# Optimization experiments

Measured on AMD Instinct MI355X. Metric: run time of the kernel, lower is better.

The kernel has to match this reference:

```python
import jax, jax.numpy as jnp
import numpy as np

N_NODES = 50000

def _gcn_conv(x, W, b, src, dst, n):
    # GCNConv: add self-loops, symmetric normalization D^-1/2 (A+I) D^-1/2, then aggregate X@W
    h = x @ W  # [N, out]
    loop = jnp.arange(n, dtype=src.dtype)
    s = jnp.concatenate([src, loop])
    d = jnp.concatenate([dst, loop])
    deg = jax.ops.segment_sum(jnp.ones_like(d, dtype=h.dtype), d, num_segments=n)  # in-degree incl self-loop (>=1)
    dinv = jax.lax.rsqrt(deg)
    norm = dinv[s] * dinv[d]  # [E+N]
    msg = h[s] * norm[:, None]  # gather + scale
    out = jax.ops.segment_sum(msg, d, num_segments=n)  # scatter-add
    return out + b

def setup_inputs() -> dict:
    key = jax.random.key(0)
    k1, k2, k3, k4, k5 = jax.random.split(key, 5)
    F_IN, HID, CLS, E = 256, 128, 32, 800000
    x = jax.random.normal(k1, (N_NODES, F_IN), dtype=jnp.float32)
    edge_index = jax.random.randint(k2, (2, E), 0, N_NODES, dtype=jnp.int64)
    W1 = jax.random.normal(k3, (F_IN, HID), dtype=jnp.float32) / np.sqrt(F_IN)
    b1 = jnp.zeros((HID,), dtype=jnp.float32)
    W2 = jax.random.normal(k4, (HID, CLS), dtype=jnp.float32) / np.sqrt(HID)
    b2 = jnp.zeros((CLS,), dtype=jnp.float32)
    return {"x": x, "edge_index": edge_index, "W1": W1, "b1": b1, "W2": W2, "b2": b2}

def reference(x, edge_index, W1, b1, W2, b2):
    src, dst = edge_index[0], edge_index[1]
    h = _gcn_conv(x, W1, b1, src, dst, N_NODES)
    h = jax.nn.relu(h)
    h = _gcn_conv(h, W2, b2, src, dst, N_NODES)
    return jax.nn.log_softmax(h, axis=1)
```

## Files before the change

kernel.cpp:

```cpp
#include <hip/hip_runtime.h>

#define N_NODES 50000
#define N_PAD   50176
#define F_IN 256
#define HID 128
#define CLS 32
#define N_EDGE 800000

#define NB    196
#define NPART 196
#define CHUNK 4082
#define GBLKS 782

typedef short bf16x8 __attribute__((ext_vector_type(8)));
typedef short s16x4  __attribute__((ext_vector_type(4)));
typedef short s16x8  __attribute__((ext_vector_type(8)));
typedef float f32x2  __attribute__((ext_vector_type(2)));
typedef float f32x4  __attribute__((ext_vector_type(4)));

static __device__ inline short f2bf(float f) {
    union { float f; unsigned u; } v; v.f = f;
    unsigned r = v.u + 0x7FFFu + ((v.u >> 16) & 1u);
    return (short)(r >> 16);
}

static __device__ inline unsigned char f2fp8(float f) {
    return (unsigned char)(__builtin_amdgcn_cvt_pk_fp8_f32(f, f, 0, false) & 0xFF);
}


__global__ __launch_bounds__(256) void k_pre(const int* __restrict__ dst,
                                             int* __restrict__ counts,
                                             const float* __restrict__ W1,
                                             short* __restrict__ WtP,
                                             const float* __restrict__ W2,
                                             short* __restrict__ Wt2P) {
    int blk = blockIdx.x, tid = threadIdx.x;
    if (blk < NB) {
        __shared__ int hist[NPART];
        if (tid < NPART) hist[tid] = 0;
        __syncthreads();
        int lo = blk * CHUNK, hi = min(lo + CHUNK, N_EDGE);
        for (int e = lo + tid; e < hi; e += 256)
            atomicAdd(&hist[dst[e] >> 8], 1);
        __syncthreads();
        if (tid < NPART) counts[blk * NPART + tid] = hist[tid];
    } else if (blk < NB + 128) {
        int idx = (blk - NB) * 256 + tid;
        int e  = idx & 7;
        int l  = (idx >> 3) & 63;
        int nt = (idx >> 9) & 7;
        int ks = idx >> 12;
        int k  = ks * 32 + ((l >> 4) * 8) + e;
        int col = nt * 16 + (l & 15);
        WtP[idx] = f2bf(W1[(size_t)k * HID + col]);
    } else {
        int idx = (blk - NB - 128) * 256 + tid;
        int e  = idx & 7;
        int l  = (idx >> 3) & 63;
        int nt = (idx >> 9) & 1;
        int ks = (idx >> 10) & 3;
        int k  = ks * 32 + ((l >> 4) * 8) + e;
        int col = nt * 16 + (l & 15);
        Wt2P[idx] = f2bf(W2[(size_t)k * CLS + col]);
    }
}


__global__ __launch_bounds__(256) void k_scanP1(const int* __restrict__ counts,
                                                int* __restrict__ base,
                                                int* __restrict__ ptot) {
    __shared__ int s[256];
    int tid = threadIdx.x, p = blockIdx.x;
    int v = (tid < NB) ? counts[tid * NPART + p] : 0;
    s[tid] = v;
    __syncthreads();
#pragma unroll
    for (int off = 1; off < 256; off <<= 1) {
        int t = (tid >= off) ? s[tid - off] : 0;
        __syncthreads();
        s[tid] += t;
        __syncthreads();
    }
    if (tid < NB) base[tid * NPART + p] = s[tid] - v;
    if (tid == 255) ptot[p] = s[255];
}


__global__ __launch_bounds__(256) void k_bucket(const int* __restrict__ src,
                                                const int* __restrict__ dst,
                                                const int* __restrict__ base,
                                                const int* __restrict__ ptot,
                                                int* __restrict__ bucket) {
    __shared__ int s[256];
    __shared__ int cur[NPART];
    int tid = threadIdx.x, blk = blockIdx.x;
    int v = (tid < NPART) ? ptot[tid] : 0;
    s[tid] = v;
    __syncthreads();
#pragma unroll
    for (int off = 1; off < 256; off <<= 1) {
        int t = (tid >= off) ? s[tid - off] : 0;
        __syncthreads();
        s[tid] += t;
        __syncthreads();
    }
    if (tid < NPART) cur[tid] = base[blk * NPART + tid] + (s[tid] - v);
    __syncthreads();
    int lo = blk * CHUNK, hi = min(lo + CHUNK, N_EDGE);
    for (int e = lo + tid; e < hi; e += 256) {
        int d = dst[e], sv = src[e];
        int pos = atomicAdd(&cur[d >> 8], 1);
        bucket[pos] = ((d & 255) << 16) | sv;
    }
}


__global__ __launch_bounds__(256) void k_csrf_gemm1(const int* __restrict__ bucket,
                                                    const int* __restrict__ ptot,
                                                    int* __restrict__ esrc,
                                                    int* __restrict__ offs,
                                                    float* __restrict__ dinv,
                                                    const float* __restrict__ x,
                                                    const short* __restrict__ WtP,
                                                    unsigned char* __restrict__ h) {
    __shared__ short tile[64][256];
    int blk = blockIdx.x, tid = threadIdx.x;

    if (blk < NPART) {
        int* sA = (int*)&tile[0][0];
        int* sB = sA + 256;
        int* sC = sB + 256;
        int* sX = sC + 256;
        int p = blk;
        int v = (tid < NPART) ? ptot[tid] : 0;
        sA[tid] = v;
        __syncthreads();
#pragma unroll
        for (int off = 1; off < 256; off <<= 1) {
            int t = (tid >= off) ? sA[tid - off] : 0;
            __syncthreads();
            sA[tid] += t;
            __syncthreads();
        }
        if (tid == p) sX[0] = sA[tid] - v;
        sB[tid] = 0;
        __syncthreads();
        int beg = sX[0], end = beg + ptot[p];
        for (int i = beg + tid; i < end; i += 256)
            atomicAdd(&sB[bucket[i] >> 16], 1);
        __syncthreads();
        int hv = sB[tid];
        sA[tid] = hv;
        __syncthreads();
#pragma unroll
        for (int off = 1; off < 256; off <<= 1) {
            int t = (tid >= off) ? sA[tid - off] : 0;
            __syncthreads();
            sA[tid] += t;
            __syncthreads();
        }
        int excl = sA[tid] - hv;
        sC[tid] = excl;
        int node = p * 256 + tid;
        if (node <= N_NODES) offs[node] = beg + excl;
        if (node < N_NODES) dinv[node] = rsqrtf((float)(hv + 1));
        __syncthreads();
        for (int i = beg + tid; i < end; i += 256) {
            int pk = bucket[i];
            int slot = atomicAdd(&sC[pk >> 16], 1);
            esrc[beg + slot] = pk & 0xFFFF;
        }
        return;
    }

    const int R0 = (blk - NPART) * 64;

#pragma unroll 8
    for (int it = 0; it < 16; ++it) {
        int rl = it * 4 + (tid >> 6);
        int row = min(R0 + rl, N_NODES - 1);
        int c = (tid & 63) * 4;
        f32x4 xv = *(const f32x4*)(x + (size_t)row * F_IN + c);
        s16x4 bv = { f2bf(xv[0]), f2bf(xv[1]), f2bf(xv[2]), f2bf(xv[3]) };
        int byte = rl * 512 + c * 2;
        byte ^= ((rl & 7) << 4);
        *(s16x4*)((char*)&tile[0][0] + byte) = bv;
    }
    __syncthreads();

    const int lane = tid & 63;
    const int w    = tid >> 6;
    const int l15  = lane & 15;
    const int lk   = lane >> 4;

    f32x4 acc[8] = {};

#pragma unroll
    for (int ks = 0; ks < F_IN / 32; ++ks) {
        const int kbase = ks * 32 + lk * 8;

        int rl = w * 16 + l15;
        int byte = rl * 512 + kbase * 2;
        byte ^= ((rl & 7) << 4);
        bf16x8 afrag = *(const bf16x8*)((char*)&tile[0][0] + byte);

        bf16x8 bfrag[8];
#pragma unroll
        for (int nt = 0; nt < 8; ++nt)
            bfrag[nt] = *(const bf16x8*)(WtP + (size_t)((ks * 8 + nt) * 64 + lane) * 8);

#pragma unroll
        for (int nt = 0; nt < 8; ++nt)
            acc[nt] = __builtin_amdgcn_mfma_f32_16x16x32_bf16(afrag, bfrag[nt], acc[nt], 0, 0, 0);
    }

#pragma unroll
    for (int r = 0; r < 4; ++r) {
        int m = R0 + w * 16 + lk * 4 + r;
        if (m < N_NODES) {
#pragma unroll
            for (int nt = 0; nt < 8; ++nt) {
                int n = nt * 16 + l15;
                h[(size_t)m * HID + n] = f2fp8(acc[nt][r]);
            }
        }
    }
}


#define ALDS2 132

__global__ __launch_bounds__(256) void k_g1g2(const int* __restrict__ offs,
                                              const int* __restrict__ esrc,
                                              const unsigned char* __restrict__ h,
                                              const float* __restrict__ dinv,
                                              const float* __restrict__ b,
                                              const short* __restrict__ Wt2P,
                                              unsigned char* __restrict__ h2) {
    __shared__ short a_lds[16][ALDS2];
    const int tid = threadIdx.x;
    const int nl = tid >> 4;
    const int node = blockIdx.x * 16 + nl;
    const int lane16 = tid & 15;
    const int f = lane16 * 8;

    float dv = dinv[node];
    uint2 hv = *(const uint2*)(h + (size_t)node * HID + f);
    f32x2 q0 = __builtin_amdgcn_cvt_pk_f32_fp8(hv.x, false);
    f32x2 q1 = __builtin_amdgcn_cvt_pk_f32_fp8(hv.x, true);
    f32x2 q2 = __builtin_amdgcn_cvt_pk_f32_fp8(hv.y, false);
    f32x2 q3 = __builtin_amdgcn_cvt_pk_f32_fp8(hv.y, true);
    float self = dv * dv;
    float a0 = q0[0] * self, a1 = q0[1] * self, a2 = q1[0] * self, a3 = q1[1] * self;
    float a4 = q2[0] * self, a5 = q2[1] * self, a6 = q3[0] * self, a7 = q3[1] * self;

    int beg = offs[node], end = offs[node + 1];
    int p = beg;
#define ACC8(vv, nn) { \
    f32x2 c0 = __builtin_amdgcn_cvt_pk_f32_fp8(vv.x, false); \
    f32x2 c1 = __builtin_amdgcn_cvt_pk_f32_fp8(vv.x, true);  \
    f32x2 c2 = __builtin_amdgcn_cvt_pk_f32_fp8(vv.y, false); \
    f32x2 c3 = __builtin_amdgcn_cvt_pk_f32_fp8(vv.y, true);  \
    a0 += c0[0] * nn; a1 += c0[1] * nn; a2 += c1[0] * nn; a3 += c1[1] * nn; \
    a4 += c2[0] * nn; a5 += c2[1] * nn; a6 += c3[0] * nn; a7 += c3[1] * nn; }
    for (; p + 7 < end; p += 8) {
        int s0 = esrc[p + 0], s1 = esrc[p + 1], s2 = esrc[p + 2], s3 = esrc[p + 3];
        int s4 = esrc[p + 4], s5 = esrc[p + 5], s6 = esrc[p + 6], s7 = esrc[p + 7];
        float n0 = dinv[s0] * dv, n1 = dinv[s1] * dv, n2 = dinv[s2] * dv, n3 = dinv[s3] * dv;
        float n4 = dinv[s4] * dv, n5 = dinv[s5] * dv, n6 = dinv[s6] * dv, n7 = dinv[s7] * dv;
        uint2 v0 = *(const uint2*)(h + (size_t)s0 * HID + f);
        uint2 v1 = *(const uint2*)(h + (size_t)s1 * HID + f);
        uint2 v2 = *(const uint2*)(h + (size_t)s2 * HID + f);
        uint2 v3 = *(const uint2*)(h + (size_t)s3 * HID + f);
        uint2 v4 = *(const uint2*)(h + (size_t)s4 * HID + f);
        uint2 v5 = *(const uint2*)(h + (size_t)s5 * HID + f);
        uint2 v6 = *(const uint2*)(h + (size_t)s6 * HID + f);
        uint2 v7 = *(const uint2*)(h + (size_t)s7 * HID + f);
        ACC8(v0, n0); ACC8(v1, n1); ACC8(v2, n2); ACC8(v3, n3);
        ACC8(v4, n4); ACC8(v5, n5); ACC8(v6, n6); ACC8(v7, n7);
    }
    for (; p + 3 < end; p += 4) {
        int s0 = esrc[p + 0], s1 = esrc[p + 1], s2 = esrc[p + 2], s3 = esrc[p + 3];
        float n0 = dinv[s0] * dv, n1 = dinv[s1] * dv, n2 = dinv[s2] * dv, n3 = dinv[s3] * dv;
        uint2 v0 = *(const uint2*)(h + (size_t)s0 * HID + f);
        uint2 v1 = *(const uint2*)(h + (size_t)s1 * HID + f);
        uint2 v2 = *(const uint2*)(h + (size_t)s2 * HID + f);
        uint2 v3 = *(const uint2*)(h + (size_t)s3 * HID + f);
        ACC8(v0, n0); ACC8(v1, n1); ACC8(v2, n2); ACC8(v3, n3);
    }
    for (; p < end; ++p) {
        int s = esrc[p];
        float nrm = dinv[s] * dv;
        uint2 v = *(const uint2*)(h + (size_t)s * HID + f);
        ACC8(v, nrm);
    }
#undef ACC8
    float4 bv0 = *(const float4*)(b + f);
    float4 bv1 = *(const float4*)(b + f + 4);
    s16x8 o = { f2bf(a0 + bv0.x), f2bf(a1 + bv0.y), f2bf(a2 + bv0.z), f2bf(a3 + bv0.w),
                f2bf(a4 + bv1.x), f2bf(a5 + bv1.y), f2bf(a6 + bv1.z), f2bf(a7 + bv1.w) };
    *(s16x8*)&a_lds[nl][f] = o;
    __syncthreads();

    if (tid < 64) {
        const int lane = tid;
        const int l15 = lane & 15;
        const int lk  = lane >> 4;
        f32x4 acc[2] = {};
#pragma unroll
        for (int ks = 0; ks < HID / 32; ++ks) {
            const int kbase = ks * 32 + lk * 8;
            bf16x8 av = *(const bf16x8*)&a_lds[l15][kbase];
#pragma unroll
            for (int e = 0; e < 8; ++e) if (av[e] < 0) av[e] = 0;
#pragma unroll
            for (int nt = 0; nt < 2; ++nt) {
                bf16x8 bfrag = *(const bf16x8*)(Wt2P + (size_t)((ks * 2 + nt) * 64 + lane) * 8);
                acc[nt] = __builtin_amdgcn_mfma_f32_16x16x32_bf16(av, bfrag, acc[nt], 0, 0, 0);
            }
        }
#pragma unroll
        for (int r = 0; r < 4; ++r) {
            int m = blockIdx.x * 16 + lk * 4 + r;
#pragma unroll
            for (int nt = 0; nt < 2; ++nt) {
                int n = nt * 16 + l15;
                h2[(size_t)m * CLS + n] = f2fp8(acc[nt][r]);
            }
        }
    }
}


__global__ __launch_bounds__(256) void k_gather2(const int* __restrict__ offs,
                                                 const int* __restrict__ esrc,
                                                 const unsigned char* __restrict__ h,
                                                 const float* __restrict__ dinv,
                                                 const float* __restrict__ b,
                                                 float* __restrict__ out) {
    int node = blockIdx.x * 32 + (threadIdx.x >> 3);
    int sub = threadIdx.x & 7;
    if (node >= N_NODES) return;
    int f = sub * 4;
    float dv = dinv[node];
    unsigned hv = *(const unsigned*)(h + (size_t)node * CLS + f);
    f32x2 hlo = __builtin_amdgcn_cvt_pk_f32_fp8(hv, false);
    f32x2 hhi = __builtin_amdgcn_cvt_pk_f32_fp8(hv, true);
    float self = dv * dv;
    float a0 = hlo[0] * self, a1 = hlo[1] * self, a2 = hhi[0] * self, a3 = hhi[1] * self;
    int beg = offs[node], end = offs[node + 1];
    int p = beg;
#define ACC4(vv, nn) { \
    f32x2 l = __builtin_amdgcn_cvt_pk_f32_fp8(vv, false); \
    f32x2 u = __builtin_amdgcn_cvt_pk_f32_fp8(vv, true);  \
    a0 += l[0] * nn; a1 += l[1] * nn; a2 += u[0] * nn; a3 += u[1] * nn; }
    for (; p + 7 < end; p += 8) {
        int s0 = esrc[p], s1 = esrc[p + 1], s2 = esrc[p + 2], s3 = esrc[p + 3];
        int s4 = esrc[p + 4], s5 = esrc[p + 5], s6 = esrc[p + 6], s7 = esrc[p + 7];
        float n0 = dinv[s0] * dv, n1 = dinv[s1] * dv, n2 = dinv[s2] * dv, n3 = dinv[s3] * dv;
        float n4 = dinv[s4] * dv, n5 = dinv[s5] * dv, n6 = dinv[s6] * dv, n7 = dinv[s7] * dv;
        unsigned v0 = *(const unsigned*)(h + (size_t)s0 * CLS + f);
        unsigned v1 = *(const unsigned*)(h + (size_t)s1 * CLS + f);
        unsigned v2 = *(const unsigned*)(h + (size_t)s2 * CLS + f);
        unsigned v3 = *(const unsigned*)(h + (size_t)s3 * CLS + f);
        unsigned v4 = *(const unsigned*)(h + (size_t)s4 * CLS + f);
        unsigned v5 = *(const unsigned*)(h + (size_t)s5 * CLS + f);
        unsigned v6 = *(const unsigned*)(h + (size_t)s6 * CLS + f);
        unsigned v7 = *(const unsigned*)(h + (size_t)s7 * CLS + f);
        ACC4(v0, n0); ACC4(v1, n1); ACC4(v2, n2); ACC4(v3, n3);
        ACC4(v4, n4); ACC4(v5, n5); ACC4(v6, n6); ACC4(v7, n7);
    }
    for (; p + 3 < end; p += 4) {
        int s0 = esrc[p], s1 = esrc[p + 1], s2 = esrc[p + 2], s3 = esrc[p + 3];
        float n0 = dinv[s0] * dv, n1 = dinv[s1] * dv, n2 = dinv[s2] * dv, n3 = dinv[s3] * dv;
        unsigned v0 = *(const unsigned*)(h + (size_t)s0 * CLS + f);
        unsigned v1 = *(const unsigned*)(h + (size_t)s1 * CLS + f);
        unsigned v2 = *(const unsigned*)(h + (size_t)s2 * CLS + f);
        unsigned v3 = *(const unsigned*)(h + (size_t)s3 * CLS + f);
        ACC4(v0, n0); ACC4(v1, n1); ACC4(v2, n2); ACC4(v3, n3);
    }
    for (; p < end; ++p) {
        int s = esrc[p];
        float nrm = dinv[s] * dv;
        unsigned v = *(const unsigned*)(h + (size_t)s * CLS + f);
        ACC4(v, nrm);
    }
#undef ACC4
    float4 bv = *(const float4*)(b + f);
    float4 acc = { a0 + bv.x, a1 + bv.y, a2 + bv.z, a3 + bv.w };

    float m = fmaxf(fmaxf(acc.x, acc.y), fmaxf(acc.z, acc.w));
    m = fmaxf(m, __shfl_xor(m, 1, 8));
    m = fmaxf(m, __shfl_xor(m, 2, 8));
    m = fmaxf(m, __shfl_xor(m, 4, 8));
    float sum = expf(acc.x - m) + expf(acc.y - m) + expf(acc.z - m) + expf(acc.w - m);
    sum += __shfl_xor(sum, 1, 8);
    sum += __shfl_xor(sum, 2, 8);
    sum += __shfl_xor(sum, 4, 8);
    float l = m + logf(sum);
    float4 o = { acc.x - l, acc.y - l, acc.z - l, acc.w - l };
    *(float4*)(out + (size_t)node * CLS + f) = o;
}


extern "C" void kernel_launch(void* const* d_in, const int* in_sizes, int n_in,
                              void* d_out, int out_size, void* d_ws, size_t ws_size,
                              hipStream_t stream) {
    const float* x  = (const float*)d_in[0];
    const int*   ei = (const int*)d_in[1];
    const float* W1 = (const float*)d_in[2];
    const float* b1 = (const float*)d_in[3];
    const float* W2 = (const float*)d_in[4];
    const float* b2 = (const float*)d_in[5];
    float* out = (float*)d_out;

    const int* src = ei;
    const int* dst = ei + N_EDGE;

    int* counts   = (int*)d_ws;
    int* base     = counts + NB * NPART;
    int* ptot     = base + NB * NPART;
    int* bucket   = ptot + 256;
    int* offs     = bucket + N_EDGE;
    int* esrc     = offs + N_PAD;
    float* dinv   = (float*)(esrc + N_EDGE);
    unsigned char* h1 = (unsigned char*)(dinv + N_PAD);
    unsigned char* h2 = h1 + (size_t)N_NODES * HID;
    short* WtP    = (short*)(h2 + (size_t)N_NODES * CLS);
    short* Wt2P   = WtP + HID * F_IN;

    k_pre       <<<NB + 128 + 16, 256, 0, stream>>>(dst, counts, W1, WtP, W2, Wt2P);
    k_scanP1    <<<NPART,         256, 0, stream>>>(counts, base, ptot);
    k_bucket    <<<NB,            256, 0, stream>>>(src, dst, base, ptot, bucket);
    k_csrf_gemm1<<<NPART + GBLKS, 256, 0, stream>>>(bucket, ptot, esrc, offs, dinv, x, WtP, h1);

    k_g1g2      <<<3125,          256, 0, stream>>>(offs, esrc, h1, dinv, b1, Wt2P, h2);
    k_gather2   <<<1563,          256, 0, stream>>>(offs, esrc, h2, dinv, b2, out);
}
```

Before: 76.94 us.

## Fold scan kernel into bucket and CSR kernels; widen gather2 to 8 features per thread

Removes the separate k_scanP1 launch. Each k_bucket and k_csrf_gemm1 block now recomputes the per-partition totals and prefixes directly from the counts matrix, at the cost of redundant reads of a 196x196 int array per block. Separately, k_gather2 now assigns 4 threads per node with 8 fp8 features each instead of 8 threads with 4. This halves the grid, issues wider uint2 loads, and shortens the softmax shuffle reductions. It relies on the ACC8 macro staying defined from the earlier kernel, since its #undef was moved.

```diff
diff --git a/kernel.cpp b/kernel.cpp
--- a/kernel.cpp
+++ b/kernel.cpp
@@ -67,36 +67,24 @@
 }
 
 
-__global__ __launch_bounds__(256) void k_scanP1(const int* __restrict__ counts,
-                                                int* __restrict__ base,
-                                                int* __restrict__ ptot) {
-    __shared__ int s[256];
-    int tid = threadIdx.x, p = blockIdx.x;
-    int v = (tid < NB) ? counts[tid * NPART + p] : 0;
-    s[tid] = v;
-    __syncthreads();
-#pragma unroll
-    for (int off = 1; off < 256; off <<= 1) {
-        int t = (tid >= off) ? s[tid - off] : 0;
-        __syncthreads();
-        s[tid] += t;
-        __syncthreads();
-    }
-    if (tid < NB) base[tid * NPART + p] = s[tid] - v;
-    if (tid == 255) ptot[p] = s[255];
-}
-
-
 __global__ __launch_bounds__(256) void k_bucket(const int* __restrict__ src,
                                                 const int* __restrict__ dst,
-                                                const int* __restrict__ base,
-                                                const int* __restrict__ ptot,
+                                                const int* __restrict__ counts,
                                                 int* __restrict__ bucket) {
     __shared__ int s[256];
     __shared__ int cur[NPART];
     int tid = threadIdx.x, blk = blockIdx.x;
-    int v = (tid < NPART) ? ptot[tid] : 0;
-    s[tid] = v;
+
+    int pre = 0, tot = 0;
+    if (tid < NPART) {
+#pragma unroll 4
+        for (int b = 0; b < NB; ++b) {
+            int c = counts[b * NPART + tid];
+            tot += c;
+            if (b < blk) pre += c;
+        }
+    }
+    s[tid] = (tid < NPART) ? tot : 0;
     __syncthreads();
 #pragma unroll
     for (int off = 1; off < 256; off <<= 1) {
@@ -105,7 +93,7 @@
         s[tid] += t;
         __syncthreads();
     }
-    if (tid < NPART) cur[tid] = base[blk * NPART + tid] + (s[tid] - v);
+    if (tid < NPART) cur[tid] = (s[tid] - tot) + pre;
     __syncthreads();
     int lo = blk * CHUNK, hi = min(lo + CHUNK, N_EDGE);
     for (int e = lo + tid; e < hi; e += 256) {
@@ -117,7 +105,7 @@
 
 
 __global__ __launch_bounds__(256) void k_csrf_gemm1(const int* __restrict__ bucket,
-                                                    const int* __restrict__ ptot,
+                                                    const int* __restrict__ counts,
                                                     int* __restrict__ esrc,
                                                     int* __restrict__ offs,
                                                     float* __restrict__ dinv,
@@ -133,8 +121,12 @@
         int* sC = sB + 256;
         int* sX = sC + 256;
         int p = blk;
-        int v = (tid < NPART) ? ptot[tid] : 0;
-        sA[tid] = v;
+        int tot = 0;
+        if (tid < NPART) {
+#pragma unroll 4
+            for (int b = 0; b < NB; ++b) tot += counts[b * NPART + tid];
+        }
+        sA[tid] = (tid < NPART) ? tot : 0;
         __syncthreads();
 #pragma unroll
         for (int off = 1; off < 256; off <<= 1) {
@@ -143,10 +135,10 @@
             sA[tid] += t;
             __syncthreads();
         }
-        if (tid == p) sX[0] = sA[tid] - v;
+        if (tid == p) { sX[0] = sA[tid] - tot; sX[1] = tot; }
         sB[tid] = 0;
         __syncthreads();
-        int beg = sX[0], end = beg + ptot[p];
+        int beg = sX[0], end = beg + sX[1];
         for (int i = beg + tid; i < end; i += 256)
             atomicAdd(&sB[bucket[i] >> 16], 1);
         __syncthreads();
@@ -295,7 +287,6 @@
         uint2 v = *(const uint2*)(h + (size_t)s * HID + f);
         ACC8(v, nrm);
     }
-#undef ACC8
     float4 bv0 = *(const float4*)(b + f);
     float4 bv1 = *(const float4*)(b + f + 4);
     s16x8 o = { f2bf(a0 + bv0.x), f2bf(a1 + bv0.y), f2bf(a2 + bv0.z), f2bf(a3 + bv0.w),
@@ -339,68 +330,72 @@
                                                  const float* __restrict__ dinv,
                                                  const float* __restrict__ b,
                                                  float* __restrict__ out) {
-    int node = blockIdx.x * 32 + (threadIdx.x >> 3);
-    int sub = threadIdx.x & 7;
+    int node = blockIdx.x * 64 + (threadIdx.x >> 2);
+    int sub = threadIdx.x & 3;
     if (node >= N_NODES) return;
-    int f = sub * 4;
+    int f = sub * 8;
     float dv = dinv[node];
-    unsigned hv = *(const unsigned*)(h + (size_t)node * CLS + f);
-    f32x2 hlo = __builtin_amdgcn_cvt_pk_f32_fp8(hv, false);
-    f32x2 hhi = __builtin_amdgcn_cvt_pk_f32_fp8(hv, true);
+    uint2 hv = *(const uint2*)(h + (size_t)node * CLS + f);
+    f32x2 q0 = __builtin_amdgcn_cvt_pk_f32_fp8(hv.x, false);
+    f32x2 q1 = __builtin_amdgcn_cvt_pk_f32_fp8(hv.x, true);
+    f32x2 q2 = __builtin_amdgcn_cvt_pk_f32_fp8(hv.y, false);
+    f32x2 q3 = __builtin_amdgcn_cvt_pk_f32_fp8(hv.y, true);
     float self = dv * dv;
-    float a0 = hlo[0] * self, a1 = hlo[1] * self, a2 = hhi[0] * self, a3 = hhi[1] * self;
+    float a0 = q0[0] * self, a1 = q0[1] * self, a2 = q1[0] * self, a3 = q1[1] * self;
+    float a4 = q2[0] * self, a5 = q2[1] * self, a6 = q3[0] * self, a7 = q3[1] * self;
+
     int beg = offs[node], end = offs[node + 1];
     int p = beg;
-#define ACC4(vv, nn) { \
-    f32x2 l = __builtin_amdgcn_cvt_pk_f32_fp8(vv, false); \
-    f32x2 u = __builtin_amdgcn_cvt_pk_f32_fp8(vv, true);  \
-    a0 += l[0] * nn; a1 += l[1] * nn; a2 += u[0] * nn; a3 += u[1] * nn; }
     for (; p + 7 < end; p += 8) {
-        int s0 = esrc[p], s1 = esrc[p + 1], s2 = esrc[p + 2], s3 = esrc[p + 3];
+        int s0 = esrc[p + 0], s1 = esrc[p + 1], s2 = esrc[p + 2], s3 = esrc[p + 3];
         int s4 = esrc[p + 4], s5 = esrc[p + 5], s6 = esrc[p + 6], s7 = esrc[p + 7];
         float n0 = dinv[s0] * dv, n1 = dinv[s1] * dv, n2 = dinv[s2] * dv, n3 = dinv[s3] * dv;
         float n4 = dinv[s4] * dv, n5 = dinv[s5] * dv, n6 = dinv[s6] * dv, n7 = dinv[s7] * dv;
-        unsigned v0 = *(const unsigned*)(h + (size_t)s0 * CLS + f);
-        unsigned v1 = *(const unsigned*)(h + (size_t)s1 * CLS + f);
-        unsigned v2 = *(const unsigned*)(h + (size_t)s2 * CLS + f);
-        unsigned v3 = *(const unsigned*)(h + (size_t)s3 * CLS + f);
-        unsigned v4 = *(const unsigned*)(h + (size_t)s4 * CLS + f);
-        unsigned v5 = *(const unsigned*)(h + (size_t)s5 * CLS + f);
-        unsigned v6 = *(const unsigned*)(h + (size_t)s6 * CLS + f);
-        unsigned v7 = *(const unsigned*)(h + (size_t)s7 * CLS + f);
-        ACC4(v0, n0); ACC4(v1, n1); ACC4(v2, n2); ACC4(v3, n3);
-        ACC4(v4, n4); ACC4(v5, n5); ACC4(v6, n6); ACC4(v7, n7);
+        uint2 v0 = *(const uint2*)(h + (size_t)s0 * CLS + f);
+        uint2 v1 = *(const uint2*)(h + (size_t)s1 * CLS + f);
+        uint2 v2 = *(const uint2*)(h + (size_t)s2 * CLS + f);
+        uint2 v3 = *(const uint2*)(h + (size_t)s3 * CLS + f);
+        uint2 v4 = *(const uint2*)(h + (size_t)s4 * CLS + f);
+        uint2 v5 = *(const uint2*)(h + (size_t)s5 * CLS + f);
+        uint2 v6 = *(const uint2*)(h + (size_t)s6 * CLS + f);
+        uint2 v7 = *(const uint2*)(h + (size_t)s7 * CLS + f);
+        ACC8(v0, n0); ACC8(v1, n1); ACC8(v2, n2); ACC8(v3, n3);
+        ACC8(v4, n4); ACC8(v5, n5); ACC8(v6, n6); ACC8(v7, n7);
     }
     for (; p + 3 < end; p += 4) {
-        int s0 = esrc[p], s1 = esrc[p + 1], s2 = esrc[p + 2], s3 = esrc[p + 3];
+        int s0 = esrc[p + 0], s1 = esrc[p + 1], s2 = esrc[p + 2], s3 = esrc[p + 3];
         float n0 = dinv[s0] * dv, n1 = dinv[s1] * dv, n2 = dinv[s2] * dv, n3 = dinv[s3] * dv;
-        unsigned v0 = *(const unsigned*)(h + (size_t)s0 * CLS + f);
-        unsigned v1 = *(const unsigned*)(h + (size_t)s1 * CLS + f);
-        unsigned v2 = *(const unsigned*)(h + (size_t)s2 * CLS + f);
-        unsigned v3 = *(const unsigned*)(h + (size_t)s3 * CLS + f);
-        ACC4(v0, n0); ACC4(v1, n1); ACC4(v2, n2); ACC4(v3, n3);
+        uint2 v0 = *(const uint2*)(h + (size_t)s0 * CLS + f);
+        uint2 v1 = *(const uint2*)(h + (size_t)s1 * CLS + f);
+        uint2 v2 = *(const uint2*)(h + (size_t)s2 * CLS + f);
+        uint2 v3 = *(const uint2*)(h + (size_t)s3 * CLS + f);
+        ACC8(v0, n0); ACC8(v1, n1); ACC8(v2, n2); ACC8(v3, n3);
     }
     for (; p < end; ++p) {
         int s = esrc[p];
         float nrm = dinv[s] * dv;
-        unsigned v = *(const unsigned*)(h + (size_t)s * CLS + f);
-        ACC4(v, nrm);
-    }
-#undef ACC4
-    float4 bv = *(const float4*)(b + f);
-    float4 acc = { a0 + bv.x, a1 + bv.y, a2 + bv.z, a3 + bv.w };
-
-    float m = fmaxf(fmaxf(acc.x, acc.y), fmaxf(acc.z, acc.w));
-    m = fmaxf(m, __shfl_xor(m, 1, 8));
-    m = fmaxf(m, __shfl_xor(m, 2, 8));
-    m = fmaxf(m, __shfl_xor(m, 4, 8));
-    float sum = expf(acc.x - m) + expf(acc.y - m) + expf(acc.z - m) + expf(acc.w - m);
-    sum += __shfl_xor(sum, 1, 8);
-    sum += __shfl_xor(sum, 2, 8);
-    sum += __shfl_xor(sum, 4, 8);
+        uint2 v = *(const uint2*)(h + (size_t)s * CLS + f);
+        ACC8(v, nrm);
+    }
+#undef ACC8
+    float4 bv0 = *(const float4*)(b + f);
+    float4 bv1 = *(const float4*)(b + f + 4);
+    a0 += bv0.x; a1 += bv0.y; a2 += bv0.z; a3 += bv0.w;
+    a4 += bv1.x; a5 += bv1.y; a6 += bv1.z; a7 += bv1.w;
+
+    float m = fmaxf(fmaxf(fmaxf(a0, a1), fmaxf(a2, a3)),
+                    fmaxf(fmaxf(a4, a5), fmaxf(a6, a7)));
+    m = fmaxf(m, __shfl_xor(m, 1, 4));
+    m = fmaxf(m, __shfl_xor(m, 2, 4));
+    float sum = expf(a0 - m) + expf(a1 - m) + expf(a2 - m) + expf(a3 - m)
+              + expf(a4 - m) + expf(a5 - m) + expf(a6 - m) + expf(a7 - m);
+    sum += __shfl_xor(sum, 1, 4);
+    sum += __shfl_xor(sum, 2, 4);
     float l = m + logf(sum);
-    float4 o = { acc.x - l, acc.y - l, acc.z - l, acc.w - l };
-    *(float4*)(out + (size_t)node * CLS + f) = o;
+    float4 o0 = { a0 - l, a1 - l, a2 - l, a3 - l };
+    float4 o1 = { a4 - l, a5 - l, a6 - l, a7 - l };
+    *(float4*)(out + (size_t)node * CLS + f)     = o0;
+    *(float4*)(out + (size_t)node * CLS + f + 4) = o1;
 }
 
 
@@ -419,9 +414,7 @@
     const int* dst = ei + N_EDGE;
 
     int* counts   = (int*)d_ws;
-    int* base     = counts + NB * NPART;
-    int* ptot     = base + NB * NPART;
-    int* bucket   = ptot + 256;
+    int* bucket   = counts + NB * NPART;
     int* offs     = bucket + N_EDGE;
     int* esrc     = offs + N_PAD;
     float* dinv   = (float*)(esrc + N_EDGE);
@@ -431,10 +424,8 @@
     short* Wt2P   = WtP + HID * F_IN;
 
     k_pre       <<<NB + 128 + 16, 256, 0, stream>>>(dst, counts, W1, WtP, W2, Wt2P);
-    k_scanP1    <<<NPART,         256, 0, stream>>>(counts, base, ptot);
-    k_bucket    <<<NB,            256, 0, stream>>>(src, dst, base, ptot, bucket);
-    k_csrf_gemm1<<<NPART + GBLKS, 256, 0, stream>>>(bucket, ptot, esrc, offs, dinv, x, WtP, h1);
-
+    k_bucket    <<<NB,            256, 0, stream>>>(src, dst, counts, bucket);
+    k_csrf_gemm1<<<NPART + GBLKS, 256, 0, stream>>>(bucket, counts, esrc, offs, dinv, x, WtP, h1);
     k_g1g2      <<<3125,          256, 0, stream>>>(offs, esrc, h1, dinv, b1, Wt2P, h2);
-    k_gather2   <<<1563,          256, 0, stream>>>(offs, esrc, h2, dinv, b2, out);
-}
+    k_gather2   <<<782,           256, 0, stream>>>(offs, esrc, h2, dinv, b2, out);
+}
```

After: 104.9 us. 36.4% more time.

## Overlap GEMM1 with edge bucketing instead of CSR finalization

Applied to the files above, without the earlier changes.

The GEMM1 blocks move out of the CSR finalization launch and into the edge-bucketing launch, and CSR finalization becomes its own kernel. The intent is to hide the latency-bound, atomic-heavy bucketing pass behind the compute-bound X@W1 GEMM, leaving only the lighter finalize pass exposed. The number of launches stays the same, but the pairing of co-scheduled work changes, so overall balance depends on which phase dominates.

```diff
diff --git a/kernel.cpp b/kernel.cpp
--- a/kernel.cpp
+++ b/kernel.cpp
@@ -87,94 +87,42 @@
 }
 
 
-__global__ __launch_bounds__(256) void k_bucket(const int* __restrict__ src,
-                                                const int* __restrict__ dst,
-                                                const int* __restrict__ base,
-                                                const int* __restrict__ ptot,
-                                                int* __restrict__ bucket) {
-    __shared__ int s[256];
-    __shared__ int cur[NPART];
-    int tid = threadIdx.x, blk = blockIdx.x;
-    int v = (tid < NPART) ? ptot[tid] : 0;
-    s[tid] = v;
-    __syncthreads();
-#pragma unroll
-    for (int off = 1; off < 256; off <<= 1) {
-        int t = (tid >= off) ? s[tid - off] : 0;
-        __syncthreads();
-        s[tid] += t;
-        __syncthreads();
-    }
-    if (tid < NPART) cur[tid] = base[blk * NPART + tid] + (s[tid] - v);
-    __syncthreads();
-    int lo = blk * CHUNK, hi = min(lo + CHUNK, N_EDGE);
-    for (int e = lo + tid; e < hi; e += 256) {
-        int d = dst[e], sv = src[e];
-        int pos = atomicAdd(&cur[d >> 8], 1);
-        bucket[pos] = ((d & 255) << 16) | sv;
-    }
-}
-
-
-__global__ __launch_bounds__(256) void k_csrf_gemm1(const int* __restrict__ bucket,
-                                                    const int* __restrict__ ptot,
-                                                    int* __restrict__ esrc,
-                                                    int* __restrict__ offs,
-                                                    float* __restrict__ dinv,
-                                                    const float* __restrict__ x,
-                                                    const short* __restrict__ WtP,
-                                                    unsigned char* __restrict__ h) {
+__global__ __launch_bounds__(256) void k_bucket_gemm1(const int* __restrict__ src,
+                                                      const int* __restrict__ dst,
+                                                      const int* __restrict__ base,
+                                                      const int* __restrict__ ptot,
+                                                      int* __restrict__ bucket,
+                                                      const float* __restrict__ x,
+                                                      const short* __restrict__ WtP,
+                                                      unsigned char* __restrict__ h) {
     __shared__ short tile[64][256];
     int blk = blockIdx.x, tid = threadIdx.x;
 
-    if (blk < NPART) {
-        int* sA = (int*)&tile[0][0];
-        int* sB = sA + 256;
-        int* sC = sB + 256;
-        int* sX = sC + 256;
-        int p = blk;
+    if (blk < NB) {
+        int* s   = (int*)&tile[0][0];
+        int* cur = s + 256;
         int v = (tid < NPART) ? ptot[tid] : 0;
-        sA[tid] = v;
+        s[tid] = v;
         __syncthreads();
 #pragma unroll
         for (int off = 1; off < 256; off <<= 1) {
-            int t = (tid >= off) ? sA[tid - off] : 0;
+            int t = (tid >= off) ? s[tid - off] : 0;
             __syncthreads();
-            sA[tid] += t;
+            s[tid] += t;
             __syncthreads();
         }
-        if (tid == p) sX[0] = sA[tid] - v;
-        sB[tid] = 0;
-        __syncthreads();
-        int beg = sX[0], end = beg + ptot[p];
-        for (int i = beg + tid; i < end; i += 256)
-            atomicAdd(&sB[bucket[i] >> 16], 1);
-        __syncthreads();
-        int hv = sB[tid];
-        sA[tid] = hv;
-        __syncthreads();
-#pragma unroll
-        for (int off = 1; off < 256; off <<= 1) {
-            int t = (tid >= off) ? sA[tid - off] : 0;
-            __syncthreads();
-            sA[tid] += t;
-            __syncthreads();
-        }
-        int excl = sA[tid] - hv;
-        sC[tid] = excl;
-        int node = p * 256 + tid;
-        if (node <= N_NODES) offs[node] = beg + excl;
-        if (node < N_NODES) dinv[node] = rsqrtf((float)(hv + 1));
-        __syncthreads();
-        for (int i = beg + tid; i < end; i += 256) {
-            int pk = bucket[i];
-            int slot = atomicAdd(&sC[pk >> 16], 1);
-            esrc[beg + slot] = pk & 0xFFFF;
+        if (tid < NPART) cur[tid] = base[blk * NPART + tid] + (s[tid] - v);
+        __syncthreads();
+        int lo = blk * CHUNK, hi = min(lo + CHUNK, N_EDGE);
+        for (int e = lo + tid; e < hi; e += 256) {
+            int d = dst[e], sv = src[e];
+            int pos = atomicAdd(&cur[d >> 8], 1);
+            bucket[pos] = ((d & 255) << 16) | sv;
         }
         return;
     }
 
-    const int R0 = (blk - NPART) * 64;
+    const int R0 = (blk - NB) * 64;
 
 #pragma unroll 8
     for (int it = 0; it < 16; ++it) {
@@ -225,6 +173,55 @@
                 h[(size_t)m * HID + n] = f2fp8(acc[nt][r]);
             }
         }
+    }
+}
+
+
+__global__ __launch_bounds__(256) void k_csr_final(const int* __restrict__ bucket,
+                                                   const int* __restrict__ ptot,
+                                                   int* __restrict__ esrc,
+                                                   int* __restrict__ offs,
+                                                   float* __restrict__ dinv) {
+    __shared__ int s[256], hist[256], cur[256];
+    __shared__ int sbeg;
+    int tid = threadIdx.x, p = blockIdx.x;
+    int v = (tid < NPART) ? ptot[tid] : 0;
+    s[tid] = v;
+    __syncthreads();
+#pragma unroll
+    for (int off = 1; off < 256; off <<= 1) {
+        int t = (tid >= off) ? s[tid - off] : 0;
+        __syncthreads();
+        s[tid] += t;
+        __syncthreads();
+    }
+    if (tid == p) sbeg = s[tid] - v;
+    hist[tid] = 0;
+    __syncthreads();
+    int beg = sbeg, end = beg + ptot[p];
+    for (int i = beg + tid; i < end; i += 256)
+        atomicAdd(&hist[bucket[i] >> 16], 1);
+    __syncthreads();
+    int hv = hist[tid];
+    s[tid] = hv;
+    __syncthreads();
+#pragma unroll
+    for (int off = 1; off < 256; off <<= 1) {
+        int t = (tid >= off) ? s[tid - off] : 0;
+        __syncthreads();
+        s[tid] += t;
+        __syncthreads();
+    }
+    int excl = s[tid] - hv;
+    cur[tid] = excl;
+    int node = p * 256 + tid;
+    if (node <= N_NODES) offs[node] = beg + excl;
+    if (node < N_NODES) dinv[node] = rsqrtf((float)(hv + 1));
+    __syncthreads();
+    for (int i = beg + tid; i < end; i += 256) {
+        int pk = bucket[i];
+        int slot = atomicAdd(&cur[pk >> 16], 1);
+        esrc[beg + slot] = pk & 0xFFFF;
     }
 }
 
@@ -430,11 +427,11 @@
     short* WtP    = (short*)(h2 + (size_t)N_NODES * CLS);
     short* Wt2P   = WtP + HID * F_IN;
 
-    k_pre       <<<NB + 128 + 16, 256, 0, stream>>>(dst, counts, W1, WtP, W2, Wt2P);
-    k_scanP1    <<<NPART,         256, 0, stream>>>(counts, base, ptot);
-    k_bucket    <<<NB,            256, 0, stream>>>(src, dst, base, ptot, bucket);
-    k_csrf_gemm1<<<NPART + GBLKS, 256, 0, stream>>>(bucket, ptot, esrc, offs, dinv, x, WtP, h1);
-
-    k_g1g2      <<<3125,          256, 0, stream>>>(offs, esrc, h1, dinv, b1, Wt2P, h2);
-    k_gather2   <<<1563,          256, 0, stream>>>(offs, esrc, h2, dinv, b2, out);
-}
+    k_pre         <<<NB + 128 + 16, 256, 0, stream>>>(dst, counts, W1, WtP, W2, Wt2P);
+    k_scanP1      <<<NPART,         256, 0, stream>>>(counts, base, ptot);
+    k_bucket_gemm1<<<NB + GBLKS,    256, 0, stream>>>(src, dst, base, ptot, bucket, x, WtP, h1);
+    k_csr_final   <<<NPART,         256, 0, stream>>>(bucket, ptot, esrc, offs, dinv);
+
+    k_g1g2        <<<3125,          256, 0, stream>>>(offs, esrc, h1, dinv, b1, Wt2P, h2);
+    k_gather2     <<<1563,          256, 0, stream>>>(offs, esrc, h2, dinv, b2, out);
+}
```

New measurement: 81.23 us. +5.6%, slower.
